# Performance work log

Measured on AMD Instinct MI355X. Metric: run time of the kernel, lower is better.

Reference implementation:

```python
import jax, jax.numpy as jnp
import numpy as np

N_NODES = 65536
IN_DIM = 256
HIDDEN = 256
NUM_GRAPHS = 128   # B = batch.max()+1; fixed by construction in setup_inputs
MAX_LEN = 1024     # >= max per-graph length (avg 512, binomial tail << 1024)


def _uniform(key, shape, scale):
    return jax.random.uniform(key, shape, jnp.float32, -scale, scale)


def setup_inputs() -> dict:
    key = jax.random.key(0)
    ks = jax.random.split(key, 12)
    x = jax.random.normal(ks[0], (N_NODES, IN_DIM), jnp.float32)
    batch = jnp.sort(jax.random.randint(ks[1], (N_NODES,), 0, NUM_GRAPHS)).astype(jnp.int64)
    s = 1.0 / np.sqrt(HIDDEN)  # torch nn.GRU init: U(-1/sqrt(H), 1/sqrt(H))
    # gate order follows torch: (r, z, n) stacked along first axis -> 3H rows
    params = {
        'W_ih0': _uniform(ks[2], (3 * HIDDEN, IN_DIM), s),
        'W_hh0': _uniform(ks[3], (3 * HIDDEN, HIDDEN), s),
        'b_ih0': _uniform(ks[4], (3 * HIDDEN,), s),
        'b_hh0': _uniform(ks[5], (3 * HIDDEN,), s),
        'W_ih1': _uniform(ks[6], (3 * HIDDEN, HIDDEN), s),
        'W_hh1': _uniform(ks[7], (3 * HIDDEN, HIDDEN), s),
        'b_ih1': _uniform(ks[8], (3 * HIDDEN,), s),
        'b_hh1': _uniform(ks[9], (3 * HIDDEN,), s),
    }
    return {'x': x, 'batch': batch, **params}


def _gru_layer(xs, W_ih, W_hh, b_ih, b_hh):
    # xs: [B, L, D] -> [B, L, H]; torch GRU cell math, gate order (r, z, n)
    B = xs.shape[0]
    H = W_hh.shape[1]
    gx = jnp.einsum('bld,gd->blg', xs, W_ih) + b_ih  # precompute input gates, one big GEMM

    def step(h, gx_t):
        gh = h @ W_hh.T + b_hh
        xr, xz, xn = jnp.split(gx_t, 3, axis=-1)
        hr, hz, hn = jnp.split(gh, 3, axis=-1)
        r = jax.nn.sigmoid(xr + hr)
        z = jax.nn.sigmoid(xz + hz)
        n = jnp.tanh(xn + r * hn)
        h_new = (1.0 - z) * n + z * h
        return h_new, h_new

    h0 = jnp.zeros((B, H), xs.dtype)
    _, hs = jax.lax.scan(step, h0, jnp.swapaxes(gx, 0, 1))  # [L, B, H]
    return jnp.swapaxes(hs, 0, 1)


def reference(x, batch, W_ih0, W_hh0, b_ih0, b_hh0, W_ih1, W_hh1, b_ih1, b_hh1):
    # Ragged per-graph sequences -> padded [B, MAX_LEN, D]. Padding is at the
    # end of each row; GRU is causal so valid positions match the per-graph
    # loop in the original module exactly, and the masked mean ignores padding.
    N, D = x.shape
    b32 = batch.astype(jnp.int32)
    counts = jax.ops.segment_sum(jnp.ones((N,), jnp.float32), b32, num_segments=NUM_GRAPHS)
    starts = jnp.cumsum(counts) - counts              # exclusive prefix sum
    pos = jnp.arange(N, dtype=jnp.float32) - starts[b32]
    pos = pos.astype(jnp.int32)                       # position within graph

    xp = jnp.zeros((NUM_GRAPHS, MAX_LEN, D), x.dtype).at[b32, pos].set(x)
    mask = jnp.zeros((NUM_GRAPHS, MAX_LEN), x.dtype).at[b32, pos].set(1.0)

    h = _gru_layer(xp, W_ih0, W_hh0, b_ih0, b_hh0)
    h = _gru_layer(h, W_ih1, W_hh1, b_ih1, b_hh1)

    denom = jnp.maximum(counts, 1.0)[:, None]
    out = jnp.sum(h * mask[:, :, None], axis=1) / denom  # mean over valid steps
    return out  # dropout is identity at eval
```

## Files before the change

kernel.cpp:

```cpp
#include <hip/hip_runtime.h>
#include <hip/hip_bf16.h>

typedef _Float16 half2_t __attribute__((ext_vector_type(2)));
typedef _Float16 f16x8   __attribute__((ext_vector_type(8)));
typedef float    f32x4   __attribute__((ext_vector_type(4)));
typedef unsigned short u16;
typedef unsigned int   u32;

#define N_NODES 65536
#define IN_DIM  256
#define HIDDEN  256
#define G3      768
#define NGRAPH  128

__device__ __forceinline__ float sigf(float x)    { return 1.f / (1.f + __expf(-x)); }
__device__ __forceinline__ float tanhfast(float x){ return 2.f / (1.f + __expf(-2.f * x)) - 1.f; }

__global__ void k_starts(const int* __restrict__ batch, int* __restrict__ starts, int n, int ngraph) {
    int g = blockIdx.x * blockDim.x + threadIdx.x;
    if (g > ngraph) return;
    int stride = (batch[n - 1] == 0) ? 2 : 1;
    if (g == ngraph) { starts[g] = n; return; }
    int lo = 0, hi = n;
    while (lo < hi) { int mid = (lo + hi) >> 1; if (batch[(size_t)mid * stride] < g) lo = mid + 1; else hi = mid; }
    starts[g] = lo;
}

__global__ void k_cvt8(const float* __restrict__ s, u16* __restrict__ d, int n) {
    int t = blockIdx.x * 256 + threadIdx.x;
    int i = t * 8;
    if (i >= n) return;
    float4 a = ((const float4*)(s + i))[0];
    float4 b = ((const float4*)(s + i))[1];
    f16x8 o;
    o[0] = (_Float16)a.x; o[1] = (_Float16)a.y; o[2] = (_Float16)a.z; o[3] = (_Float16)a.w;
    o[4] = (_Float16)b.x; o[5] = (_Float16)b.y; o[6] = (_Float16)b.z; o[7] = (_Float16)b.w;
    *(f16x8*)(d + i) = o;
}

__global__ void k_swz(const float* __restrict__ W, uint4* __restrict__ out) {
    int t = blockIdx.x * 256 + threadIdx.x;
    if (t >= 24576) return;
    int l = t & 63, i = (t >> 6) & 31, w = t >> 11;
    int row = w * 64 + l, col = i * 8;
    const float* s = W + row * 256 + col;
    f16x8 o;
#pragma unroll
    for (int q = 0; q < 8; q++) o[q] = (_Float16)s[q];
    out[t] = __builtin_bit_cast(uint4, o);
}

template <typename AT>
__global__ __launch_bounds__(256) void k_gemm(
    const AT* __restrict__ A, const u16* __restrict__ Bm,
    const float* __restrict__ bias, u16* __restrict__ C,
    int M, int N, int K)
{
    __shared__ u16 As[128 * 40];
    __shared__ u16 Bs[128 * 40];
    const int m0 = blockIdx.y * 128, n0 = blockIdx.x * 128;
    const int t = threadIdx.x;
    const int wave = t >> 6, lane = t & 63;
    const int wm = wave & 1, wn = wave >> 1;
    const int lr = lane & 15, lq = lane >> 4;
    f32x4 acc[4][4] = {};
    const int sr = t >> 1, sp = t & 1;
    const AT*  gA = A  + (size_t)(m0 + sr) * K + sp * 16;
    const u16* gB = Bm + (size_t)(n0 + sr) * K + sp * 16;
    u16* sA = As + sr * 40 + sp * 16;
    u16* sB = Bs + sr * 40 + sp * 16;
    for (int kt = 0; kt < K; kt += 32) {
        uint4 av0, av1;
        if constexpr (sizeof(AT) == 4) {
            float4 a0 = ((const float4*)gA)[0], a1 = ((const float4*)gA)[1];
            float4 a2 = ((const float4*)gA)[2], a3 = ((const float4*)gA)[3];
            f16x8 lo, hi;
            lo[0]=(_Float16)a0.x; lo[1]=(_Float16)a0.y; lo[2]=(_Float16)a0.z; lo[3]=(_Float16)a0.w;
            lo[4]=(_Float16)a1.x; lo[5]=(_Float16)a1.y; lo[6]=(_Float16)a1.z; lo[7]=(_Float16)a1.w;
            hi[0]=(_Float16)a2.x; hi[1]=(_Float16)a2.y; hi[2]=(_Float16)a2.z; hi[3]=(_Float16)a2.w;
            hi[4]=(_Float16)a3.x; hi[5]=(_Float16)a3.y; hi[6]=(_Float16)a3.z; hi[7]=(_Float16)a3.w;
            av0 = __builtin_bit_cast(uint4, lo);
            av1 = __builtin_bit_cast(uint4, hi);
        } else {
            av0 = ((const uint4*)gA)[0];
            av1 = ((const uint4*)gA)[1];
        }
        uint4 b0 = ((const uint4*)gB)[0], b1 = ((const uint4*)gB)[1];
        gA += 32; gB += 32;
        __syncthreads();
        ((uint4*)sA)[0] = av0; ((uint4*)sA)[1] = av1;
        ((uint4*)sB)[0] = b0;  ((uint4*)sB)[1] = b1;
        __syncthreads();
        f16x8 af[4], bf[4];
#pragma unroll
        for (int i = 0; i < 4; i++)
            af[i] = *(const f16x8*)(As + (wm * 64 + i * 16 + lr) * 40 + lq * 8);
#pragma unroll
        for (int j = 0; j < 4; j++)
            bf[j] = *(const f16x8*)(Bs + (wn * 64 + j * 16 + lr) * 40 + lq * 8);
#pragma unroll
        for (int i = 0; i < 4; i++)
#pragma unroll
            for (int j = 0; j < 4; j++)
                acc[i][j] = __builtin_amdgcn_mfma_f32_16x16x32_f16(af[i], bf[j], acc[i][j], 0, 0, 0);
    }
#pragma unroll
    for (int i = 0; i < 4; i++) {
        int row = m0 + wm * 64 + i * 16 + lq * 4;
#pragma unroll
        for (int j = 0; j < 4; j++) {
            int col = n0 + wn * 64 + j * 16 + lr;
            float bv = bias[col];
#pragma unroll
            for (int rr = 0; rr < 4; rr++) {
                _Float16 v = (_Float16)(acc[i][j][rr] + bv);
                C[(size_t)(row + rr) * N + col] = __builtin_bit_cast(u16, v);
            }
        }
    }
}

__global__ __launch_bounds__(768, 3) void k_rec(
    const u16* __restrict__ gx,
    const uint4* __restrict__ wsw,
    const float* __restrict__ bhh,
    const int*   __restrict__ starts,
    u16* __restrict__ hout,
    float* __restrict__ out)
{
    __shared__ float ghb[G3];
    __shared__ float gxb[G3];
    __shared__ uint4 hpk4[HIDDEN / 8];
    const int g = blockIdx.x;
    const int tid = threadIdx.x;
    const int start = starts[g];
    const int len = starts[g + 1] - start;
    const uint4* wp = wsw + (size_t)(tid >> 6) * 2048 + (tid & 63);
    uint4 w[32];
#pragma unroll
    for (int i = 0; i < 32; i++) w[i] = wp[(size_t)i * 64];
#pragma unroll
    for (int i = 0; i < 32; i++)
        asm volatile("" : "+v"(w[i].x), "+v"(w[i].y), "+v"(w[i].z), "+v"(w[i].w));
    const float bh = bhh[tid];
    if (tid < 32) hpk4[tid] = make_uint4(0, 0, 0, 0);
    float hp = 0.f, hs = 0.f;
    const _Float16* gxrow = (const _Float16*)gx + (size_t)start * G3 + tid;
    u16* hrow = hout ? (hout + (size_t)start * HIDDEN + tid) : (u16*)nullptr;
    __syncthreads();
    float gcur = (len > 0) ? (float)gxrow[0] : 0.f;
    for (int t = 0; t < len; ++t) {
        int tn = (t + 1 < len) ? t + 1 : t;
        float gnext = (float)gxrow[(size_t)tn * G3];
        float a0 = bh, a1 = 0.f, a2 = 0.f, a3 = 0.f;
#pragma unroll
        for (int i = 0; i < 32; i++) {
            uint4 hv = hpk4[i];
            a0 = __builtin_amdgcn_fdot2(__builtin_bit_cast(half2_t, w[i].x), __builtin_bit_cast(half2_t, hv.x), a0, false);
            a1 = __builtin_amdgcn_fdot2(__builtin_bit_cast(half2_t, w[i].y), __builtin_bit_cast(half2_t, hv.y), a1, false);
            a2 = __builtin_amdgcn_fdot2(__builtin_bit_cast(half2_t, w[i].z), __builtin_bit_cast(half2_t, hv.z), a2, false);
            a3 = __builtin_amdgcn_fdot2(__builtin_bit_cast(half2_t, w[i].w), __builtin_bit_cast(half2_t, hv.w), a3, false);
        }
        ghb[tid] = (a0 + a1) + (a2 + a3);
        gxb[tid] = gcur;
        __syncthreads();
        if (tid < HIDDEN) {
            float r = sigf(gxb[tid]       + ghb[tid]);
            float z = sigf(gxb[tid + 256] + ghb[tid + 256]);
            float n = tanhfast(gxb[tid + 512] + r * ghb[tid + 512]);
            float h = (1.f - z) * n + z * hp;
            hp = h; hs += h;
            _Float16 ph = (_Float16)h;
            u16 pk = __builtin_bit_cast(u16, ph);
            ((u16*)hpk4)[tid] = pk;
            if (hrow) hrow[(size_t)t * HIDDEN] = pk;
        }
        gcur = gnext;
        __syncthreads();
    }
    if (out && tid < HIDDEN) {
        float inv = 1.f / (float)(len > 0 ? len : 1);
        out[g * HIDDEN + tid] = hs * inv;
    }
}

extern "C" void kernel_launch(void* const* d_in, const int* in_sizes, int n_in,
                              void* d_out, int out_size, void* d_ws, size_t ws_size,
                              hipStream_t stream)
{
    const float* x     = (const float*)d_in[0];
    const int*   batch = (const int*)d_in[1];
    const float* Wih0  = (const float*)d_in[2];
    const float* Whh0  = (const float*)d_in[3];
    const float* bih0  = (const float*)d_in[4];
    const float* bhh0  = (const float*)d_in[5];
    const float* Wih1  = (const float*)d_in[6];
    const float* Whh1  = (const float*)d_in[7];
    const float* bih1  = (const float*)d_in[8];
    const float* bhh1  = (const float*)d_in[9];
    float* out = (float*)d_out;

    char* ws = (char*)d_ws;
    size_t o = 0;
    int*   starts = (int*)  (ws + o); o += 4096;
    u16*   wi0    = (u16*)  (ws + o); o += (size_t)G3 * IN_DIM * 2;
    u16*   wi1    = (u16*)  (ws + o); o += (size_t)G3 * HIDDEN * 2;
    uint4* wsw0   = (uint4*)(ws + o); o += (size_t)G3 * HIDDEN * 2;
    uint4* wsw1   = (uint4*)(ws + o); o += (size_t)G3 * HIDDEN * 2;
    u16*   h0     = (u16*)  (ws + o); o += (size_t)N_NODES * HIDDEN * 2;
    u16*   gxbuf  = (u16*)  (ws + o); o += (size_t)N_NODES * G3 * 2;

    k_starts<<<1, 256, 0, stream>>>(batch, starts, N_NODES, NGRAPH);
    k_cvt8<<<96, 256, 0, stream>>>(Wih0, wi0, G3 * IN_DIM);
    k_cvt8<<<96, 256, 0, stream>>>(Wih1, wi1, G3 * HIDDEN);
    k_swz<<<96, 256, 0, stream>>>(Whh0, wsw0);
    k_swz<<<96, 256, 0, stream>>>(Whh1, wsw1);

    k_gemm<float><<<dim3(G3 / 128, N_NODES / 128), 256, 0, stream>>>(x, wi0, bih0, gxbuf, N_NODES, G3, IN_DIM);
    k_rec<<<NGRAPH, 768, 0, stream>>>(gxbuf, wsw0, bhh0, starts, h0, (float*)nullptr);
    k_gemm<_Float16><<<dim3(G3 / 128, N_NODES / 128), 256, 0, stream>>>((const _Float16*)h0, wi1, bih1, gxbuf, N_NODES, G3, HIDDEN);
    k_rec<<<NGRAPH, 768, 0, stream>>>(gxbuf, wsw1, bhh1, starts, (u16*)nullptr, out);
}
```

Baseline: 1.690 ms.

## Compute all three gates per thread in recurrence, dropping shared gate buffers

The recurrent kernel now uses 256 threads per graph, and each thread owns one hidden unit and computes its r, z and n gate dot products itself. The W_hh swizzle is reordered so each thread's three gate rows sit contiguously. This removes the shared-memory gate exchange and one barrier-separated phase per step, and the input-gate loads are prefetched two steps ahead. In exchange each thread holds 96 uint4 weight registers (384 VGPRs) and does three times the dot-product work on a quarter of the threads, so per-step latency and register spilling are the risk.

Result: slower. 2.574 ms (+52.3%).

```diff
diff --git a/kernel.cpp b/kernel.cpp
--- a/kernel.cpp
+++ b/kernel.cpp
@@ -41,8 +41,9 @@
 __global__ void k_swz(const float* __restrict__ W, uint4* __restrict__ out) {
     int t = blockIdx.x * 256 + threadIdx.x;
     if (t >= 24576) return;
-    int l = t & 63, i = (t >> 6) & 31, w = t >> 11;
-    int row = w * 64 + l, col = i * 8;
+    int l = t & 63, i = (t >> 6) & 31, rest = t >> 11;
+    int w = rest / 3, rg = rest % 3;
+    int row = rg * 256 + w * 64 + l, col = i * 8;
     const float* s = W + row * 256 + col;
     f16x8 o;
 #pragma unroll
@@ -120,7 +121,7 @@
     }
 }
 
-__global__ __launch_bounds__(768, 3) void k_rec(
+__global__ __launch_bounds__(256, 1) void k_rec(
     const u16* __restrict__ gx,
     const uint4* __restrict__ wsw,
     const float* __restrict__ bhh,
@@ -128,57 +129,73 @@
     u16* __restrict__ hout,
     float* __restrict__ out)
 {
-    __shared__ float ghb[G3];
-    __shared__ float gxb[G3];
     __shared__ uint4 hpk4[HIDDEN / 8];
     const int g = blockIdx.x;
     const int tid = threadIdx.x;
+    const int wv = tid >> 6, l = tid & 63;
     const int start = starts[g];
     const int len = starts[g + 1] - start;
-    const uint4* wp = wsw + (size_t)(tid >> 6) * 2048 + (tid & 63);
-    uint4 w[32];
-#pragma unroll
-    for (int i = 0; i < 32; i++) w[i] = wp[(size_t)i * 64];
-#pragma unroll
-    for (int i = 0; i < 32; i++)
-        asm volatile("" : "+v"(w[i].x), "+v"(w[i].y), "+v"(w[i].z), "+v"(w[i].w));
-    const float bh = bhh[tid];
+    uint4 w[3][32];
+#pragma unroll
+    for (int rg = 0; rg < 3; rg++)
+#pragma unroll
+        for (int i = 0; i < 32; i++)
+            w[rg][i] = wsw[(size_t)((wv * 3 + rg) * 32 + i) * 64 + l];
+    const float bhr = bhh[tid], bhz = bhh[tid + 256], bhn = bhh[tid + 512];
     if (tid < 32) hpk4[tid] = make_uint4(0, 0, 0, 0);
     float hp = 0.f, hs = 0.f;
-    const _Float16* gxrow = (const _Float16*)gx + (size_t)start * G3 + tid;
+    const _Float16* gxr = (const _Float16*)gx + (size_t)start * G3 + tid;
     u16* hrow = hout ? (hout + (size_t)start * HIDDEN + tid) : (u16*)nullptr;
     __syncthreads();
-    float gcur = (len > 0) ? (float)gxrow[0] : 0.f;
+    float g0r = 0, g0z = 0, g0n = 0, g1r = 0, g1z = 0, g1n = 0;
+    if (len > 0) {
+        g0r = (float)gxr[0]; g0z = (float)gxr[256]; g0n = (float)gxr[512];
+        size_t o1 = (size_t)(len > 1 ? 1 : 0) * G3;
+        g1r = (float)gxr[o1]; g1z = (float)gxr[o1 + 256]; g1n = (float)gxr[o1 + 512];
+    }
     for (int t = 0; t < len; ++t) {
-        int tn = (t + 1 < len) ? t + 1 : t;
-        float gnext = (float)gxrow[(size_t)tn * G3];
-        float a0 = bh, a1 = 0.f, a2 = 0.f, a3 = 0.f;
+        int tp = t + 2 < len ? t + 2 : len - 1;
+        size_t op = (size_t)tp * G3;
+        float g2r = (float)gxr[op], g2z = (float)gxr[op + 256], g2n = (float)gxr[op + 512];
+        float ar0 = bhr, ar1 = 0.f, ar2 = 0.f, ar3 = 0.f;
+        float az0 = bhz, az1 = 0.f, az2 = 0.f, az3 = 0.f;
+        float an0 = bhn, an1 = 0.f, an2 = 0.f, an3 = 0.f;
 #pragma unroll
         for (int i = 0; i < 32; i++) {
             uint4 hv = hpk4[i];
-            a0 = __builtin_amdgcn_fdot2(__builtin_bit_cast(half2_t, w[i].x), __builtin_bit_cast(half2_t, hv.x), a0, false);
-            a1 = __builtin_amdgcn_fdot2(__builtin_bit_cast(half2_t, w[i].y), __builtin_bit_cast(half2_t, hv.y), a1, false);
-            a2 = __builtin_amdgcn_fdot2(__builtin_bit_cast(half2_t, w[i].z), __builtin_bit_cast(half2_t, hv.z), a2, false);
-            a3 = __builtin_amdgcn_fdot2(__builtin_bit_cast(half2_t, w[i].w), __builtin_bit_cast(half2_t, hv.w), a3, false);
+            half2_t hx = __builtin_bit_cast(half2_t, hv.x), hy = __builtin_bit_cast(half2_t, hv.y);
+            half2_t hz = __builtin_bit_cast(half2_t, hv.z), hw = __builtin_bit_cast(half2_t, hv.w);
+            ar0 = __builtin_amdgcn_fdot2(__builtin_bit_cast(half2_t, w[0][i].x), hx, ar0, false);
+            ar1 = __builtin_amdgcn_fdot2(__builtin_bit_cast(half2_t, w[0][i].y), hy, ar1, false);
+            ar2 = __builtin_amdgcn_fdot2(__builtin_bit_cast(half2_t, w[0][i].z), hz, ar2, false);
+            ar3 = __builtin_amdgcn_fdot2(__builtin_bit_cast(half2_t, w[0][i].w), hw, ar3, false);
+            az0 = __builtin_amdgcn_fdot2(__builtin_bit_cast(half2_t, w[1][i].x), hx, az0, false);
+            az1 = __builtin_amdgcn_fdot2(__builtin_bit_cast(half2_t, w[1][i].y), hy, az1, false);
+            az2 = __builtin_amdgcn_fdot2(__builtin_bit_cast(half2_t, w[1][i].z), hz, az2, false);
+            az3 = __builtin_amdgcn_fdot2(__builtin_bit_cast(half2_t, w[1][i].w), hw, az3, false);
+            an0 = __builtin_amdgcn_fdot2(__builtin_bit_cast(half2_t, w[2][i].x), hx, an0, false);
+            an1 = __builtin_amdgcn_fdot2(__builtin_bit_cast(half2_t, w[2][i].y), hy, an1, false);
+            an2 = __builtin_amdgcn_fdot2(__builtin_bit_cast(half2_t, w[2][i].z), hz, an2, false);
+            an3 = __builtin_amdgcn_fdot2(__builtin_bit_cast(half2_t, w[2][i].w), hw, an3, false);
         }
-        ghb[tid] = (a0 + a1) + (a2 + a3);
-        gxb[tid] = gcur;
-        __syncthreads();
-        if (tid < HIDDEN) {
-            float r = sigf(gxb[tid]       + ghb[tid]);
-            float z = sigf(gxb[tid + 256] + ghb[tid + 256]);
-            float n = tanhfast(gxb[tid + 512] + r * ghb[tid + 512]);
-            float h = (1.f - z) * n + z * hp;
-            hp = h; hs += h;
-            _Float16 ph = (_Float16)h;
-            u16 pk = __builtin_bit_cast(u16, ph);
-            ((u16*)hpk4)[tid] = pk;
-            if (hrow) hrow[(size_t)t * HIDDEN] = pk;
-        }
-        gcur = gnext;
-        __syncthreads();
-    }
-    if (out && tid < HIDDEN) {
+        float ghr = (ar0 + ar1) + (ar2 + ar3);
+        float ghz = (az0 + az1) + (az2 + az3);
+        float ghn = (an0 + an1) + (an2 + an3);
+        float r = sigf(g0r + ghr);
+        float z = sigf(g0z + ghz);
+        float n = tanhfast(g0n + r * ghn);
+        float h = (1.f - z) * n + z * hp;
+        hp = h; hs += h;
+        _Float16 ph = (_Float16)h;
+        u16 pk = __builtin_bit_cast(u16, ph);
+        __syncthreads();
+        ((u16*)hpk4)[tid] = pk;
+        if (hrow) hrow[(size_t)t * HIDDEN] = pk;
+        g0r = g1r; g0z = g1z; g0n = g1n;
+        g1r = g2r; g1z = g2z; g1n = g2n;
+        __syncthreads();
+    }
+    if (out) {
         float inv = 1.f / (float)(len > 0 ? len : 1);
         out[g * HIDDEN + tid] = hs * inv;
     }
@@ -217,7 +234,7 @@
     k_swz<<<96, 256, 0, stream>>>(Whh1, wsw1);
 
     k_gemm<float><<<dim3(G3 / 128, N_NODES / 128), 256, 0, stream>>>(x, wi0, bih0, gxbuf, N_NODES, G3, IN_DIM);
-    k_rec<<<NGRAPH, 768, 0, stream>>>(gxbuf, wsw0, bhh0, starts, h0, (float*)nullptr);
+    k_rec<<<NGRAPH, 256, 0, stream>>>(gxbuf, wsw0, bhh0, starts, h0, (float*)nullptr);
     k_gemm<_Float16><<<dim3(G3 / 128, N_NODES / 128), 256, 0, stream>>>((const _Float16*)h0, wi1, bih1, gxbuf, N_NODES, G3, HIDDEN);
-    k_rec<<<NGRAPH, 768, 0, stream>>>(gxbuf, wsw1, bhh1, starts, (u16*)nullptr, out);
-}
+    k_rec<<<NGRAPH, 256, 0, stream>>>(gxbuf, wsw1, bhh1, starts, (u16*)nullptr, out);
+}
```
